# Kernel tuning notes

Hardware: AMD Instinct MI355X
Metric: run time of the kernel (lower is better)

## Reference

```python
import jax, jax.numpy as jnp
import numpy as np

B, IN, OUT = 4096, 1024, 1024
HALF_PI = np.pi / 2.0
TWO_PI = 2.0 * np.pi
# cyclic control-point index table per quadrant (from the torch module)
CPI = jnp.array([[3, 0, 1, 2], [0, 1, 2, 3], [1, 2, 3, 0], [2, 3, 0, 1]], dtype=jnp.int32)
# Catmull-Rom cubic spline basis (4 control points, [t^3,t^2,t,1] monomials)
BASIS = np.array([[-0.5, 1.5, -1.5, 0.5],
                  [1.0, -2.5, 2.0, -0.5],
                  [-0.5, 0.0, 0.5, 0.0],
                  [0.0, 1.0, 0.0, 0.0]], dtype=np.float32)


def setup_inputs() -> dict:
    key = jax.random.key(0)
    k_x, k_p, k_w, k_b = jax.random.split(key, 4)
    x = jax.random.normal(k_x, (B, IN), dtype=jnp.float32)
    phase = jax.random.uniform(k_p, (B,), dtype=jnp.float32) * TWO_PI
    # kaiming_uniform_(a=sqrt(5)) on each (OUT, IN) slice -> bound = 1/sqrt(fan_in)
    bound = 1.0 / np.sqrt(IN)
    weights = jax.random.uniform(k_w, (4, OUT, IN), dtype=jnp.float32, minval=-bound, maxval=bound)
    biases = jax.random.uniform(k_b, (4, OUT), dtype=jnp.float32, minval=-bound, maxval=bound)
    basis = jnp.asarray(BASIS)
    return {"input": x, "phase": phase, "weights": weights, "biases": biases, "basis": basis}


def reference(input, phase, weights, biases, basis):
    # quadrant index q in {0,1,2,3}; same selection as the nested torch.where chain
    q = jnp.clip(jnp.floor(phase / HALF_PI).astype(jnp.int32), 0, 3)          # (B,)
    t = phase / HALF_PI - q.astype(phase.dtype)                                # (B,), in [0,1)
    tt = jnp.stack([t ** 3, t ** 2, t, jnp.ones_like(t)], axis=-1)             # (B,4)
    coeffs = tt @ basis                                                        # (B,4) spline coeffs
    idx = CPI[q]                                                               # (B,4) control-point ids
    # Instead of materializing per-sample (B,OUT,IN) weights, contract input against
    # all 4 control-point matrices (same math: w_b = sum_k c_k W_{idx_k}).
    z = jnp.einsum('bi,coi->bco', input, weights)                              # (B,4,OUT)
    zg = jnp.take_along_axis(z, idx[:, :, None], axis=1)                       # (B,4,OUT)
    bg = biases[idx]                                                           # (B,4,OUT)
    return jnp.einsum('bk,bko->bo', coeffs, zg + bg)                           # (B,OUT)
```

## Files before the change

### kernel.cpp

```cpp
#include <hip/hip_runtime.h>
#include <stdint.h>

#define BATCH   4096
#define IN_DIM  1024
#define OUT_DIM 1024

typedef __bf16 bf16x8 __attribute__((ext_vector_type(8)));
typedef float  f32x4  __attribute__((ext_vector_type(4)));

__device__ __forceinline__ uint16_t f2bf(float f) {
    union { float f; uint32_t u; } v; v.f = f;
    uint32_t u = v.u;
    uint32_t r = (u + 0x7FFFu + ((u >> 16) & 1u)) >> 16;
    return (uint16_t)r;
}

__device__ __forceinline__ float bf2f(uint16_t h) {
    union { uint32_t u; float f; } v; v.u = ((uint32_t)h) << 16;
    return v.f;
}

__global__ __launch_bounds__(256) void prep(
    const float* __restrict__ x, const float* __restrict__ phase,
    const float* __restrict__ basis, const float* __restrict__ W,
    uint16_t* __restrict__ xb, uint16_t* __restrict__ Wb,
    float* __restrict__ alphaWS)
{
    const int bid = blockIdx.x;
    const int tid = threadIdx.x;

    if (bid < BATCH) {
        const int b = bid;
        const float HALF_PI = 1.5707963267948966f;
        float s  = phase[b] / HALF_PI;
        int   q  = (int)floorf(s);
        q = q < 0 ? 0 : (q > 3 ? 3 : q);
        float t  = s - (float)q;
        float t2 = t * t, t3 = t2 * t;

        float coef[4];
#pragma unroll
        for (int j = 0; j < 4; ++j)
            coef[j] = t3 * basis[j] + t2 * basis[4 + j] + t * basis[8 + j] + basis[12 + j];

        if (tid < 4) alphaWS[b * 4 + tid] = coef[(tid - q + 1) & 3];

        float4 xv = ((const float4*)(x + (size_t)b * IN_DIM))[tid];
        ushort4 o;
        o.x = f2bf(xv.x); o.y = f2bf(xv.y); o.z = f2bf(xv.z); o.w = f2bf(xv.w);
        ((ushort4*)(xb + (size_t)b * IN_DIM))[tid] = o;
    } else {
        const int j = bid - BATCH;
        float4 wv = ((const float4*)W)[j * 256 + tid];
        ushort4 o;
        o.x = f2bf(wv.x); o.y = f2bf(wv.y); o.z = f2bf(wv.z); o.w = f2bf(wv.w);
        ((ushort4*)Wb)[j * 256 + tid] = o;
    }
}

__global__ __launch_bounds__(256, 4) void gemm_split(
    const uint16_t* __restrict__ xb, const uint16_t* __restrict__ Wb,
    uint16_t* __restrict__ P)
{
    __shared__ uint16_t As[128 * 64];
    __shared__ uint16_t Bs[128 * 64];

    const int tid  = threadIdx.x;
    const int lane = tid & 63;
    const int wid  = tid >> 6;
    const int wm   = wid >> 1;
    const int wn   = wid & 1;
    const int tileM = blockIdx.x * 128;
    const int tileN = blockIdx.y * 128;
    const int c     = blockIdx.z;

    f32x4 acc[4][4];
#pragma unroll
    for (int mi = 0; mi < 4; ++mi)
#pragma unroll
        for (int ni = 0; ni < 4; ++ni)
            acc[mi][ni] = (f32x4){0.f, 0.f, 0.f, 0.f};

    const int srow = lane >> 3;
    const int gchunk = ((lane & 7) ^ srow) * 8;

    const uint16_t* Ag = xb + (size_t)tileM * 1024;
    const uint16_t* Bg = Wb + ((size_t)c << 20) + (size_t)tileN * 1024;

    const int quad = lane >> 4;
    const int l7   = lane & 7;

    for (int kt = 0; kt < 16; ++kt) {
        const int k0 = kt * 64;
#pragma unroll
        for (int j = 0; j < 4; ++j) {
            const int s = wid * 4 + j;
            const uint16_t* ga = Ag + (size_t)(s * 8 + srow) * 1024 + k0 + gchunk;
            __builtin_amdgcn_global_load_lds(
                (const __attribute__((address_space(1))) void*)ga,
                (__attribute__((address_space(3))) void*)(As + s * 512), 16, 0, 0);
            const uint16_t* gb = Bg + (size_t)(s * 8 + srow) * 1024 + k0 + gchunk;
            __builtin_amdgcn_global_load_lds(
                (const __attribute__((address_space(1))) void*)gb,
                (__attribute__((address_space(3))) void*)(Bs + s * 512), 16, 0, 0);
        }
        __syncthreads();

#pragma unroll
        for (int ks = 0; ks < 2; ++ks) {
            bf16x8 af[4], bfr[4];
#pragma unroll
            for (int mi = 0; mi < 4; ++mi) {
                const int row = wm * 64 + mi * 16 + (lane & 15);
                const int ch  = (ks * 4 + quad) ^ l7;
                af[mi] = *(const bf16x8*)(As + row * 64 + ch * 8);
            }
#pragma unroll
            for (int ni = 0; ni < 4; ++ni) {
                const int row = wn * 64 + ni * 16 + (lane & 15);
                const int ch  = (ks * 4 + quad) ^ l7;
                bfr[ni] = *(const bf16x8*)(Bs + row * 64 + ch * 8);
            }
#pragma unroll
            for (int mi = 0; mi < 4; ++mi)
#pragma unroll
                for (int ni = 0; ni < 4; ++ni)
                    acc[mi][ni] = __builtin_amdgcn_mfma_f32_16x16x32_bf16(
                        af[mi], bfr[ni], acc[mi][ni], 0, 0, 0);
        }
        __syncthreads();
    }

    uint16_t* Pc = P + (size_t)c * (BATCH * (size_t)OUT_DIM);
    const int col0 = tileN + wn * 64 + (lane & 15);
#pragma unroll
    for (int mi = 0; mi < 4; ++mi) {
#pragma unroll
        for (int r = 0; r < 4; ++r) {
            const int m = tileM + wm * 64 + mi * 16 + quad * 4 + r;
#pragma unroll
            for (int ni = 0; ni < 4; ++ni)
                Pc[(size_t)m * OUT_DIM + col0 + ni * 16] = f2bf(acc[mi][ni][r]);
        }
    }
}

__global__ __launch_bounds__(256) void reduce_k(
    const uint16_t* __restrict__ P, const float* __restrict__ alphaWS,
    const float* __restrict__ biases, float* __restrict__ out)
{
    const int m = blockIdx.x;
    const int t = threadIdx.x;
    const size_t stride = (size_t)BATCH * OUT_DIM;

    const float4 al = *(const float4*)(alphaWS + 4 * m);
    float4 r = {0.f, 0.f, 0.f, 0.f};
    const float a[4] = {al.x, al.y, al.z, al.w};
#pragma unroll
    for (int c = 0; c < 4; ++c) {
        ushort4 p = ((const ushort4*)(P + c * stride + (size_t)m * OUT_DIM))[t];
        float4 b  = ((const float4*)(biases + c * OUT_DIM))[t];
        r.x += a[c] * (bf2f(p.x) + b.x);
        r.y += a[c] * (bf2f(p.y) + b.y);
        r.z += a[c] * (bf2f(p.z) + b.z);
        r.w += a[c] * (bf2f(p.w) + b.w);
    }
    ((float4*)(out + (size_t)m * OUT_DIM))[t] = r;
}

extern "C" void kernel_launch(void* const* d_in, const int* in_sizes, int n_in,
                              void* d_out, int out_size, void* d_ws, size_t ws_size,
                              hipStream_t stream)
{
    const float* x       = (const float*)d_in[0];
    const float* phase   = (const float*)d_in[1];
    const float* weights = (const float*)d_in[2];
    const float* biases  = (const float*)d_in[3];
    const float* basis   = (const float*)d_in[4];
    float* out = (float*)d_out;

    uint16_t* xb = (uint16_t*)d_ws;
    uint16_t* Wb = xb + (size_t)BATCH * IN_DIM;
    float* alphaWS = (float*)(Wb + (size_t)4 * OUT_DIM * IN_DIM);
    uint16_t* P = (uint16_t*)(alphaWS + (size_t)BATCH * 4);

    prep<<<2 * BATCH, 256, 0, stream>>>(x, phase, basis, weights, xb, Wb, alphaWS);

    dim3 grid(BATCH / 128, OUT_DIM / 128, 4);
    gemm_split<<<grid, 256, 0, stream>>>(xb, Wb, P);

    reduce_k<<<BATCH, 256, 0, stream>>>(P, alphaWS, biases, out);
}
```

Measured before the change: 131.1 us.

## Fold spline coefficients into K dimension and fuse reduction into single GEMM

Each input row is pre-scaled by its four per-sample spline coefficients and the copies are concatenated along K, with coefficient columns appended to pair with a bias row. A single GEMM of K=4160 then produces the final output directly, which removes the bf16 partial-product buffer and the separate reduce kernel. The tile shrinks to 128x64 so the grid keeps enough blocks. The cost is a larger prepped X, four times the A traffic per output tile, and bias and alpha now rounded to bf16.

```diff
diff --git a/kernel.cpp b/kernel.cpp
--- a/kernel.cpp
+++ b/kernel.cpp
@@ -4,6 +4,7 @@
 #define BATCH   4096
 #define IN_DIM  1024
 #define OUT_DIM 1024
+#define KDIM    4160
 
 typedef __bf16 bf16x8 __attribute__((ext_vector_type(8)));
 typedef float  f32x4  __attribute__((ext_vector_type(4)));
@@ -15,16 +16,11 @@
     return (uint16_t)r;
 }
 
-__device__ __forceinline__ float bf2f(uint16_t h) {
-    union { uint32_t u; float f; } v; v.u = ((uint32_t)h) << 16;
-    return v.f;
-}
-
 __global__ __launch_bounds__(256) void prep(
     const float* __restrict__ x, const float* __restrict__ phase,
     const float* __restrict__ basis, const float* __restrict__ W,
-    uint16_t* __restrict__ xb, uint16_t* __restrict__ Wb,
-    float* __restrict__ alphaWS)
+    const float* __restrict__ biases,
+    uint16_t* __restrict__ Xp, uint16_t* __restrict__ Wp)
 {
     const int bid = blockIdx.x;
     const int tid = threadIdx.x;
@@ -43,27 +39,45 @@
         for (int j = 0; j < 4; ++j)
             coef[j] = t3 * basis[j] + t2 * basis[4 + j] + t * basis[8 + j] + basis[12 + j];
 
-        if (tid < 4) alphaWS[b * 4 + tid] = coef[(tid - q + 1) & 3];
+        float alpha[4];
+#pragma unroll
+        for (int c = 0; c < 4; ++c)
+            alpha[c] = coef[(c - q + 1) & 3];
 
         float4 xv = ((const float4*)(x + (size_t)b * IN_DIM))[tid];
-        ushort4 o;
-        o.x = f2bf(xv.x); o.y = f2bf(xv.y); o.z = f2bf(xv.z); o.w = f2bf(xv.w);
-        ((ushort4*)(xb + (size_t)b * IN_DIM))[tid] = o;
+        uint16_t* xrow = Xp + (size_t)b * KDIM;
+#pragma unroll
+        for (int c = 0; c < 4; ++c) {
+            ushort4 o;
+            o.x = f2bf(alpha[c] * xv.x);
+            o.y = f2bf(alpha[c] * xv.y);
+            o.z = f2bf(alpha[c] * xv.z);
+            o.w = f2bf(alpha[c] * xv.w);
+            ((ushort4*)(xrow + c * IN_DIM))[tid] = o;
+        }
+        if (tid < 64)
+            xrow[4096 + tid] = (tid < 4) ? f2bf(alpha[tid]) : (uint16_t)0;
     } else {
-        const int j = bid - BATCH;
-        float4 wv = ((const float4*)W)[j * 256 + tid];
-        ushort4 o;
-        o.x = f2bf(wv.x); o.y = f2bf(wv.y); o.z = f2bf(wv.z); o.w = f2bf(wv.w);
-        ((ushort4*)Wb)[j * 256 + tid] = o;
+        const int n = bid - BATCH;
+        uint16_t* wrow = Wp + (size_t)n * KDIM;
+#pragma unroll
+        for (int c = 0; c < 4; ++c) {
+            float4 wv = ((const float4*)(W + ((size_t)c << 20) + (size_t)n * IN_DIM))[tid];
+            ushort4 o;
+            o.x = f2bf(wv.x); o.y = f2bf(wv.y); o.z = f2bf(wv.z); o.w = f2bf(wv.w);
+            ((ushort4*)(wrow + c * IN_DIM))[tid] = o;
+        }
+        if (tid < 64)
+            wrow[4096 + tid] = (tid < 4) ? f2bf(biases[tid * OUT_DIM + n]) : (uint16_t)0;
     }
 }
 
-__global__ __launch_bounds__(256, 4) void gemm_split(
-    const uint16_t* __restrict__ xb, const uint16_t* __restrict__ Wb,
-    uint16_t* __restrict__ P)
+__global__ __launch_bounds__(256, 2) void gemm_fused(
+    const uint16_t* __restrict__ Xp, const uint16_t* __restrict__ Wp,
+    float* __restrict__ out)
 {
     __shared__ uint16_t As[128 * 64];
-    __shared__ uint16_t Bs[128 * 64];
+    __shared__ uint16_t Bs[64 * 64];
 
     const int tid  = threadIdx.x;
     const int lane = tid & 63;
@@ -71,35 +85,38 @@
     const int wm   = wid >> 1;
     const int wn   = wid & 1;
     const int tileM = blockIdx.x * 128;
-    const int tileN = blockIdx.y * 128;
-    const int c     = blockIdx.z;
+    const int tileN = blockIdx.y * 64;
 
-    f32x4 acc[4][4];
+    f32x4 acc[4][2];
 #pragma unroll
     for (int mi = 0; mi < 4; ++mi)
 #pragma unroll
-        for (int ni = 0; ni < 4; ++ni)
+        for (int ni = 0; ni < 2; ++ni)
             acc[mi][ni] = (f32x4){0.f, 0.f, 0.f, 0.f};
 
-    const int srow = lane >> 3;
+    const int srow   = lane >> 3;
     const int gchunk = ((lane & 7) ^ srow) * 8;
 
-    const uint16_t* Ag = xb + (size_t)tileM * 1024;
-    const uint16_t* Bg = Wb + ((size_t)c << 20) + (size_t)tileN * 1024;
+    const uint16_t* Ag = Xp + (size_t)tileM * KDIM;
+    const uint16_t* Bg = Wp + (size_t)tileN * KDIM;
 
     const int quad = lane >> 4;
     const int l7   = lane & 7;
 
-    for (int kt = 0; kt < 16; ++kt) {
+    for (int kt = 0; kt < KDIM / 64; ++kt) {
         const int k0 = kt * 64;
 #pragma unroll
         for (int j = 0; j < 4; ++j) {
             const int s = wid * 4 + j;
-            const uint16_t* ga = Ag + (size_t)(s * 8 + srow) * 1024 + k0 + gchunk;
+            const uint16_t* ga = Ag + (size_t)(s * 8 + srow) * KDIM + k0 + gchunk;
             __builtin_amdgcn_global_load_lds(
                 (const __attribute__((address_space(1))) void*)ga,
                 (__attribute__((address_space(3))) void*)(As + s * 512), 16, 0, 0);
-            const uint16_t* gb = Bg + (size_t)(s * 8 + srow) * 1024 + k0 + gchunk;
+        }
+#pragma unroll
+        for (int j = 0; j < 2; ++j) {
+            const int s = wid * 2 + j;
+            const uint16_t* gb = Bg + (size_t)(s * 8 + srow) * KDIM + k0 + gchunk;
             __builtin_amdgcn_global_load_lds(
                 (const __attribute__((address_space(1))) void*)gb,
                 (__attribute__((address_space(3))) void*)(Bs + s * 512), 16, 0, 0);
@@ -108,64 +125,39 @@
 
 #pragma unroll
         for (int ks = 0; ks < 2; ++ks) {
-            bf16x8 af[4], bfr[4];
+            const int ch = (ks * 4 + quad) ^ l7;
+            bf16x8 af[4], bfr[2];
 #pragma unroll
             for (int mi = 0; mi < 4; ++mi) {
                 const int row = wm * 64 + mi * 16 + (lane & 15);
-                const int ch  = (ks * 4 + quad) ^ l7;
                 af[mi] = *(const bf16x8*)(As + row * 64 + ch * 8);
             }
 #pragma unroll
-            for (int ni = 0; ni < 4; ++ni) {
-                const int row = wn * 64 + ni * 16 + (lane & 15);
-                const int ch  = (ks * 4 + quad) ^ l7;
+            for (int ni = 0; ni < 2; ++ni) {
+                const int row = wn * 32 + ni * 16 + (lane & 15);
                 bfr[ni] = *(const bf16x8*)(Bs + row * 64 + ch * 8);
             }
 #pragma unroll
             for (int mi = 0; mi < 4; ++mi)
 #pragma unroll
-                for (int ni = 0; ni < 4; ++ni)
+                for (int ni = 0; ni < 2; ++ni)
                     acc[mi][ni] = __builtin_amdgcn_mfma_f32_16x16x32_bf16(
                         af[mi], bfr[ni], acc[mi][ni], 0, 0, 0);
         }
         __syncthreads();
     }
 
-    uint16_t* Pc = P + (size_t)c * (BATCH * (size_t)OUT_DIM);
-    const int col0 = tileN + wn * 64 + (lane & 15);
+    const int col0 = tileN + wn * 32 + (lane & 15);
 #pragma unroll
     for (int mi = 0; mi < 4; ++mi) {
 #pragma unroll
         for (int r = 0; r < 4; ++r) {
             const int m = tileM + wm * 64 + mi * 16 + quad * 4 + r;
 #pragma unroll
-            for (int ni = 0; ni < 4; ++ni)
-                Pc[(size_t)m * OUT_DIM + col0 + ni * 16] = f2bf(acc[mi][ni][r]);
+            for (int ni = 0; ni < 2; ++ni)
+                out[(size_t)m * OUT_DIM + col0 + ni * 16] = acc[mi][ni][r];
         }
     }
-}
-
-__global__ __launch_bounds__(256) void reduce_k(
-    const uint16_t* __restrict__ P, const float* __restrict__ alphaWS,
-    const float* __restrict__ biases, float* __restrict__ out)
-{
-    const int m = blockIdx.x;
-    const int t = threadIdx.x;
-    const size_t stride = (size_t)BATCH * OUT_DIM;
-
-    const float4 al = *(const float4*)(alphaWS + 4 * m);
-    float4 r = {0.f, 0.f, 0.f, 0.f};
-    const float a[4] = {al.x, al.y, al.z, al.w};
-#pragma unroll
-    for (int c = 0; c < 4; ++c) {
-        ushort4 p = ((const ushort4*)(P + c * stride + (size_t)m * OUT_DIM))[t];
-        float4 b  = ((const float4*)(biases + c * OUT_DIM))[t];
-        r.x += a[c] * (bf2f(p.x) + b.x);
-        r.y += a[c] * (bf2f(p.y) + b.y);
-        r.z += a[c] * (bf2f(p.z) + b.z);
-        r.w += a[c] * (bf2f(p.w) + b.w);
-    }
-    ((float4*)(out + (size_t)m * OUT_DIM))[t] = r;
 }
 
 extern "C" void kernel_launch(void* const* d_in, const int* in_sizes, int n_in,
@@ -179,15 +171,11 @@
     const float* basis   = (const float*)d_in[4];
     float* out = (float*)d_out;
 
-    uint16_t* xb = (uint16_t*)d_ws;
-    uint16_t* Wb = xb + (size_t)BATCH * IN_DIM;
-    float* alphaWS = (float*)(Wb + (size_t)4 * OUT_DIM * IN_DIM);
-    uint16_t* P = (uint16_t*)(alphaWS + (size_t)BATCH * 4);
+    uint16_t* Xp = (uint16_t*)d_ws;
+    uint16_t* Wp = Xp + (size_t)BATCH * KDIM;
 
-    prep<<<2 * BATCH, 256, 0, stream>>>(x, phase, basis, weights, xb, Wb, alphaWS);
+    prep<<<BATCH + OUT_DIM, 256, 0, stream>>>(x, phase, basis, weights, biases, Xp, Wp);
 
-    dim3 grid(BATCH / 128, OUT_DIM / 128, 4);
-    gemm_split<<<grid, 256, 0, stream>>>(xb, Wb, P);
-
-    reduce_k<<<BATCH, 256, 0, stream>>>(P, alphaWS, biases, out);
+    dim3 grid(BATCH / 128, OUT_DIM / 64);
+    gemm_fused<<<grid, 256, 0, stream>>>(Xp, Wp, out);
 }
```

Measured after the change: 142.4 us. 8.6% more time.

## Fuse split reduction into GEMM epilogue via fp32 atomics, init output with bias

Applied to the files above, without the earlier changes.

Removes the intermediate bf16 partial-product buffer and the separate reduction kernel. The prep kernel now writes the alpha-weighted bias sum into the output, and each control-point GEMM block atomically adds its alpha-scaled accumulator into the fp32 output. This avoids writing and re-reading a large partial buffer and one kernel launch. In exchange it uses many scalar global float atomics, which may be limited by atomic throughput and contention, and the summation order becomes nondeterministic.

```diff
diff --git a/kernel.cpp b/kernel.cpp
--- a/kernel.cpp
+++ b/kernel.cpp
@@ -15,16 +15,12 @@
     return (uint16_t)r;
 }
 
-__device__ __forceinline__ float bf2f(uint16_t h) {
-    union { uint32_t u; float f; } v; v.u = ((uint32_t)h) << 16;
-    return v.f;
-}
-
 __global__ __launch_bounds__(256) void prep(
     const float* __restrict__ x, const float* __restrict__ phase,
     const float* __restrict__ basis, const float* __restrict__ W,
+    const float* __restrict__ biases,
     uint16_t* __restrict__ xb, uint16_t* __restrict__ Wb,
-    float* __restrict__ alphaWS)
+    float* __restrict__ alphaWS, float* __restrict__ out)
 {
     const int bid = blockIdx.x;
     const int tid = threadIdx.x;
@@ -43,12 +39,28 @@
         for (int j = 0; j < 4; ++j)
             coef[j] = t3 * basis[j] + t2 * basis[4 + j] + t * basis[8 + j] + basis[12 + j];
 
-        if (tid < 4) alphaWS[b * 4 + tid] = coef[(tid - q + 1) & 3];
+        float alpha[4];
+#pragma unroll
+        for (int c = 0; c < 4; ++c)
+            alpha[c] = coef[(c - q + 1) & 3];
+
+        if (tid < 4) alphaWS[b * 4 + tid] = alpha[tid];
 
         float4 xv = ((const float4*)(x + (size_t)b * IN_DIM))[tid];
         ushort4 o;
         o.x = f2bf(xv.x); o.y = f2bf(xv.y); o.z = f2bf(xv.z); o.w = f2bf(xv.w);
         ((ushort4*)(xb + (size_t)b * IN_DIM))[tid] = o;
+
+        float4 acc = {0.f, 0.f, 0.f, 0.f};
+#pragma unroll
+        for (int c = 0; c < 4; ++c) {
+            float4 bv = ((const float4*)(biases + (size_t)c * OUT_DIM))[tid];
+            acc.x += alpha[c] * bv.x;
+            acc.y += alpha[c] * bv.y;
+            acc.z += alpha[c] * bv.z;
+            acc.w += alpha[c] * bv.w;
+        }
+        ((float4*)(out + (size_t)b * OUT_DIM))[tid] = acc;
     } else {
         const int j = bid - BATCH;
         float4 wv = ((const float4*)W)[j * 256 + tid];
@@ -60,7 +72,7 @@
 
 __global__ __launch_bounds__(256, 4) void gemm_split(
     const uint16_t* __restrict__ xb, const uint16_t* __restrict__ Wb,
-    uint16_t* __restrict__ P)
+    const float* __restrict__ alphaWS, float* __restrict__ out)
 {
     __shared__ uint16_t As[128 * 64];
     __shared__ uint16_t Bs[128 * 64];
@@ -131,41 +143,22 @@
         __syncthreads();
     }
 
-    uint16_t* Pc = P + (size_t)c * (BATCH * (size_t)OUT_DIM);
     const int col0 = tileN + wn * 64 + (lane & 15);
 #pragma unroll
     for (int mi = 0; mi < 4; ++mi) {
 #pragma unroll
         for (int r = 0; r < 4; ++r) {
-            const int m = tileM + wm * 64 + mi * 16 + quad * 4 + r;
+            const int m  = tileM + wm * 64 + mi * 16 + quad * 4 + r;
+            const float al = alphaWS[m * 4 + c];
 #pragma unroll
-            for (int ni = 0; ni < 4; ++ni)
-                Pc[(size_t)m * OUT_DIM + col0 + ni * 16] = f2bf(acc[mi][ni][r]);
+            for (int ni = 0; ni < 4; ++ni) {
+                __hip_atomic_fetch_add(
+                    &out[(size_t)m * OUT_DIM + col0 + ni * 16],
+                    al * acc[mi][ni][r],
+                    __ATOMIC_RELAXED, __HIP_MEMORY_SCOPE_AGENT);
+            }
         }
     }
-}
-
-__global__ __launch_bounds__(256) void reduce_k(
-    const uint16_t* __restrict__ P, const float* __restrict__ alphaWS,
-    const float* __restrict__ biases, float* __restrict__ out)
-{
-    const int m = blockIdx.x;
-    const int t = threadIdx.x;
-    const size_t stride = (size_t)BATCH * OUT_DIM;
-
-    const float4 al = *(const float4*)(alphaWS + 4 * m);
-    float4 r = {0.f, 0.f, 0.f, 0.f};
-    const float a[4] = {al.x, al.y, al.z, al.w};
-#pragma unroll
-    for (int c = 0; c < 4; ++c) {
-        ushort4 p = ((const ushort4*)(P + c * stride + (size_t)m * OUT_DIM))[t];
-        float4 b  = ((const float4*)(biases + c * OUT_DIM))[t];
-        r.x += a[c] * (bf2f(p.x) + b.x);
-        r.y += a[c] * (bf2f(p.y) + b.y);
-        r.z += a[c] * (bf2f(p.z) + b.z);
-        r.w += a[c] * (bf2f(p.w) + b.w);
-    }
-    ((float4*)(out + (size_t)m * OUT_DIM))[t] = r;
 }
 
 extern "C" void kernel_launch(void* const* d_in, const int* in_sizes, int n_in,
@@ -182,12 +175,10 @@
     uint16_t* xb = (uint16_t*)d_ws;
     uint16_t* Wb = xb + (size_t)BATCH * IN_DIM;
     float* alphaWS = (float*)(Wb + (size_t)4 * OUT_DIM * IN_DIM);
-    uint16_t* P = (uint16_t*)(alphaWS + (size_t)BATCH * 4);
 
-    prep<<<2 * BATCH, 256, 0, stream>>>(x, phase, basis, weights, xb, Wb, alphaWS);
+    prep<<<2 * BATCH, 256, 0, stream>>>(x, phase, basis, weights, biases,
+                                        xb, Wb, alphaWS, out);
 
     dim3 grid(BATCH / 128, OUT_DIM / 128, 4);
-    gemm_split<<<grid, 256, 0, stream>>>(xb, Wb, P);
-
-    reduce_k<<<BATCH, 256, 0, stream>>>(P, alphaWS, biases, out);
+    gemm_split<<<grid, 256, 0, stream>>>(xb, Wb, alphaWS, out);
 }
```

Result: slower. 160.1 us (+22.1%).

## Fuse spline reduction into GEMM via last-arriving-block tile counter

Applied to the files above, without the earlier changes.

Removes the separate reduce kernel. Each GEMM block bumps an atomic per-tile counter after writing its bf16 partial, and the fourth block to finish for a tile combines the four partials with the spline coefficients and biases and writes the output. This saves one kernel launch and lets the reduction overlap with GEMM work still in progress. In exchange it adds fences and atomics, and the epilogue has each thread walk a long strided row on only a quarter of the blocks, which may give uneven tail work.

```diff
diff --git a/kernel.cpp b/kernel.cpp
--- a/kernel.cpp
+++ b/kernel.cpp
@@ -24,7 +24,7 @@
     const float* __restrict__ x, const float* __restrict__ phase,
     const float* __restrict__ basis, const float* __restrict__ W,
     uint16_t* __restrict__ xb, uint16_t* __restrict__ Wb,
-    float* __restrict__ alphaWS)
+    float* __restrict__ alphaWS, int* __restrict__ tileCnt)
 {
     const int bid = blockIdx.x;
     const int tid = threadIdx.x;
@@ -51,6 +51,7 @@
         ((ushort4*)(xb + (size_t)b * IN_DIM))[tid] = o;
     } else {
         const int j = bid - BATCH;
+        if (j == 0) tileCnt[tid] = 0;
         float4 wv = ((const float4*)W)[j * 256 + tid];
         ushort4 o;
         o.x = f2bf(wv.x); o.y = f2bf(wv.y); o.z = f2bf(wv.z); o.w = f2bf(wv.w);
@@ -60,10 +61,13 @@
 
 __global__ __launch_bounds__(256, 4) void gemm_split(
     const uint16_t* __restrict__ xb, const uint16_t* __restrict__ Wb,
-    uint16_t* __restrict__ P)
+    const float* __restrict__ alphaWS, const float* __restrict__ biases,
+    uint16_t* __restrict__ P, int* __restrict__ tileCnt,
+    float* __restrict__ out)
 {
     __shared__ uint16_t As[128 * 64];
     __shared__ uint16_t Bs[128 * 64];
+    __shared__ int sLast;
 
     const int tid  = threadIdx.x;
     const int lane = tid & 63;
@@ -131,7 +135,8 @@
         __syncthreads();
     }
 
-    uint16_t* Pc = P + (size_t)c * (BATCH * (size_t)OUT_DIM);
+    const size_t stride = (size_t)BATCH * OUT_DIM;
+    uint16_t* Pc = P + (size_t)c * stride;
     const int col0 = tileN + wn * 64 + (lane & 15);
 #pragma unroll
     for (int mi = 0; mi < 4; ++mi) {
@@ -143,29 +148,41 @@
                 Pc[(size_t)m * OUT_DIM + col0 + ni * 16] = f2bf(acc[mi][ni][r]);
         }
     }
-}
-
-__global__ __launch_bounds__(256) void reduce_k(
-    const uint16_t* __restrict__ P, const float* __restrict__ alphaWS,
-    const float* __restrict__ biases, float* __restrict__ out)
-{
-    const int m = blockIdx.x;
-    const int t = threadIdx.x;
-    const size_t stride = (size_t)BATCH * OUT_DIM;
-
+
+    __threadfence();
+    __syncthreads();
+    if (tid == 0) {
+        int old = __hip_atomic_fetch_add(&tileCnt[blockIdx.y * 32 + blockIdx.x], 1,
+                                         __ATOMIC_ACQ_REL, __HIP_MEMORY_SCOPE_AGENT);
+        sLast = (old == 3);
+    }
+    __syncthreads();
+    if (!sLast) return;
+    __threadfence();
+
+    const int row = tid >> 1;
+    const int m   = tileM + row;
+    const int ch0 = (tid & 1) * 64;
     const float4 al = *(const float4*)(alphaWS + 4 * m);
-    float4 r = {0.f, 0.f, 0.f, 0.f};
     const float a[4] = {al.x, al.y, al.z, al.w};
 #pragma unroll
-    for (int c = 0; c < 4; ++c) {
-        ushort4 p = ((const ushort4*)(P + c * stride + (size_t)m * OUT_DIM))[t];
-        float4 b  = ((const float4*)(biases + c * OUT_DIM))[t];
-        r.x += a[c] * (bf2f(p.x) + b.x);
-        r.y += a[c] * (bf2f(p.y) + b.y);
-        r.z += a[c] * (bf2f(p.z) + b.z);
-        r.w += a[c] * (bf2f(p.w) + b.w);
-    }
-    ((float4*)(out + (size_t)m * OUT_DIM))[t] = r;
+    for (int g = 0; g < 16; ++g) {
+        const int col = tileN + ch0 + g * 4;
+        float4 r = {0.f, 0.f, 0.f, 0.f};
+#pragma unroll
+        for (int cc = 0; cc < 4; ++cc) {
+            unsigned long long pv = __hip_atomic_load(
+                (const unsigned long long*)(P + cc * stride + (size_t)m * OUT_DIM + col),
+                __ATOMIC_RELAXED, __HIP_MEMORY_SCOPE_AGENT);
+            ushort4 p = *(ushort4*)&pv;
+            float4 b = *(const float4*)(biases + (size_t)cc * OUT_DIM + col);
+            r.x += a[cc] * (bf2f(p.x) + b.x);
+            r.y += a[cc] * (bf2f(p.y) + b.y);
+            r.z += a[cc] * (bf2f(p.z) + b.z);
+            r.w += a[cc] * (bf2f(p.w) + b.w);
+        }
+        *(float4*)(out + (size_t)m * OUT_DIM + col) = r;
+    }
 }
 
 extern "C" void kernel_launch(void* const* d_in, const int* in_sizes, int n_in,
@@ -182,12 +199,12 @@
     uint16_t* xb = (uint16_t*)d_ws;
     uint16_t* Wb = xb + (size_t)BATCH * IN_DIM;
     float* alphaWS = (float*)(Wb + (size_t)4 * OUT_DIM * IN_DIM);
-    uint16_t* P = (uint16_t*)(alphaWS + (size_t)BATCH * 4);
-
-    prep<<<2 * BATCH, 256, 0, stream>>>(x, phase, basis, weights, xb, Wb, alphaWS);
+    int* tileCnt = (int*)(alphaWS + (size_t)BATCH * 4);
+    uint16_t* P = (uint16_t*)(tileCnt + 256);
+
+    prep<<<2 * BATCH, 256, 0, stream>>>(x, phase, basis, weights, xb, Wb,
+                                        alphaWS, tileCnt);
 
     dim3 grid(BATCH / 128, OUT_DIM / 128, 4);
-    gemm_split<<<grid, 256, 0, stream>>>(xb, Wb, P);
-
-    reduce_k<<<BATCH, 256, 0, stream>>>(P, alphaWS, biases, out);
-}
+    gemm_split<<<grid, 256, 0, stream>>>(xb, Wb, alphaWS, biases, P, tileCnt, out);
+}
```

Measured after the change: 380.4 us. +190.1%, slower.
